# Kernel optimization log

Hardware: AMD Instinct MI355X
Metric: run time of the kernel (lower is better)

## Reference

```python
import jax, jax.numpy as jnp
import numpy as np

INPUT_NC = 512
N_HEADS = 16
D_KEY = 64
SCALE = D_KEY ** 0.5


def setup_inputs() -> dict:
    key = jax.random.key(0)
    k1, k2, k3, k4, k5, k6 = jax.random.split(key, 6)
    bs, d_seq = 8, 1024
    v = jax.random.normal(k1, (bs, d_seq, INPUT_NC), dtype=jnp.float32)
    # key-padding mask, True = masked out; broadcast over heads and query dim
    pad_mask = jax.random.bernoulli(k2, 0.1, (bs, 1, 1, d_seq))
    # fc1: input_nc -> 2*n_heads*d_key (fused K,Q projection)
    W1 = jax.random.normal(k3, (INPUT_NC, 2 * N_HEADS * D_KEY), dtype=jnp.float32) * (1.0 / np.sqrt(INPUT_NC))
    b1 = jax.random.normal(k4, (2 * N_HEADS * D_KEY,), dtype=jnp.float32) * 0.01
    # fc2: n_heads*input_nc -> input_nc
    W2 = jax.random.normal(k5, (N_HEADS * INPUT_NC, INPUT_NC), dtype=jnp.float32) * (1.0 / np.sqrt(N_HEADS * INPUT_NC))
    b2 = jax.random.normal(k6, (INPUT_NC,), dtype=jnp.float32) * 0.01
    return {"v": v, "pad_mask": pad_mask, "W1": W1, "b1": b1, "W2": W2, "b2": b2}


def reference(v, pad_mask, W1, b1, W2, b2):
    bs, d_seq, nc = v.shape
    # fused KQ projection: [bs, S, 2*H*dk] -> [bs, H, S, 2*dk]
    kq = (v @ W1 + b1).reshape(bs, d_seq, N_HEADS, 2 * D_KEY).transpose(0, 2, 1, 3)
    k, q = kq[..., :D_KEY], kq[..., D_KEY:]  # chunk: k first, q second
    attn = jnp.einsum('bhqd,bhkd->bhqk', q, k) / SCALE
    attn = jnp.where(pad_mask, jnp.float32(-1000.0), attn)
    attn = jax.nn.softmax(attn, axis=3)
    # AV with unprojected v broadcast across heads: [bs, H, S, nc]
    out = jnp.einsum('bhqk,bkc->bhqc', attn, v)
    out = out.transpose(0, 2, 1, 3).reshape(bs, d_seq, N_HEADS * nc)
    out = out @ W2 + b2
    return (out, attn)
```

## Files before the change

kernel.cpp:

```cpp
#include <hip/hip_runtime.h>


typedef __attribute__((ext_vector_type(8))) short bf16x8;
typedef __attribute__((ext_vector_type(4))) float f32x4;
typedef __attribute__((ext_vector_type(4))) unsigned short u16x4;

__device__ __forceinline__ unsigned short f2bf(float f) {
  unsigned u = __builtin_bit_cast(unsigned, f);
  u += 0x7FFFu + ((u >> 16) & 1u);
  return (unsigned short)(u >> 16);
}
__device__ __forceinline__ float bf2f(unsigned short u) {
  return __builtin_bit_cast(float, (unsigned)u << 16);
}

__device__ __forceinline__ void gload_lds16(const unsigned short* g, unsigned short* l) {
  __builtin_amdgcn_global_load_lds(
      (const __attribute__((address_space(1))) unsigned int*)(g),
      (__attribute__((address_space(3))) unsigned int*)(l), 16, 0, 0);
}


__global__ void cvt_bf16_kernel(const float* __restrict__ in,
                                unsigned short* __restrict__ out, int n4) {
  int i = blockIdx.x * blockDim.x + threadIdx.x;
  if (i >= n4) return;
  f32x4 v = reinterpret_cast<const f32x4*>(in)[i];
  u16x4 o;
#pragma unroll
  for (int j = 0; j < 4; ++j) o[j] = f2bf(v[j]);
  reinterpret_cast<u16x4*>(out)[i] = o;
}

__global__ void transpose_cvt_kernel(const float* __restrict__ in,
                                     unsigned short* __restrict__ out,
                                     int R, int C) {
  __shared__ float tile[32][33];
  int c0 = blockIdx.x * 32, r0 = blockIdx.y * 32;
  int tx = threadIdx.x & 31, ty = threadIdx.x >> 5;
#pragma unroll
  for (int i = ty; i < 32; i += 8)
    tile[i][tx] = in[(size_t)(r0 + i) * C + (c0 + tx)];
  __syncthreads();
#pragma unroll
  for (int i = ty; i < 32; i += 8)
    out[(size_t)(c0 + i) * R + (r0 + tx)] = f2bf(tile[tx][i]);
}

__launch_bounds__(256)
__global__ void gemm1_kernel(const unsigned short* __restrict__ vbf,
                             const unsigned short* __restrict__ w1t,
                             const float* __restrict__ b1,
                             unsigned short* __restrict__ q_ws,
                             unsigned short* __restrict__ k_ws) {
  const int m0 = blockIdx.y * 128, n0 = blockIdx.x * 128;
  const int w = threadIdx.x >> 6, l = threadIdx.x & 63;
  const int wr = w >> 1, wc = w & 1, lr = l & 15, lg = l >> 4;
  f32x4 acc[4][4];
#pragma unroll
  for (int mi = 0; mi < 4; ++mi)
#pragma unroll
    for (int ni = 0; ni < 4; ++ni) acc[mi][ni] = (f32x4){0.f, 0.f, 0.f, 0.f};

  for (int k0 = 0; k0 < 512; k0 += 32) {
    bf16x8 a[4], bb[4];
#pragma unroll
    for (int mi = 0; mi < 4; ++mi)
      a[mi] = *reinterpret_cast<const bf16x8*>(
          vbf + (size_t)(m0 + wr * 64 + mi * 16 + lr) * 512 + k0 + lg * 8);
#pragma unroll
    for (int ni = 0; ni < 4; ++ni)
      bb[ni] = *reinterpret_cast<const bf16x8*>(
          w1t + (size_t)(n0 + wc * 64 + ni * 16 + lr) * 512 + k0 + lg * 8);
#pragma unroll
    for (int mi = 0; mi < 4; ++mi)
#pragma unroll
      for (int ni = 0; ni < 4; ++ni)
        acc[mi][ni] = __builtin_amdgcn_mfma_f32_16x16x32_bf16(a[mi], bb[ni], acc[mi][ni], 0, 0, 0);
  }
#pragma unroll
  for (int mi = 0; mi < 4; ++mi)
#pragma unroll
    for (int ni = 0; ni < 4; ++ni) {
      int col = n0 + wc * 64 + ni * 16 + lr;
      int h = col >> 7, j = col & 127;
      float bias = b1[col];
#pragma unroll
      for (int r = 0; r < 4; ++r) {
        int row = m0 + wr * 64 + mi * 16 + lg * 4 + r;
        int bb_ = row >> 10, s = row & 1023;
        unsigned short bv = f2bf(acc[mi][ni][r] + bias);
        size_t base = ((size_t)(bb_ * 16 + h) << 16) + (size_t)s * 64;
        if (j < 64) k_ws[base + j] = bv;
        else        q_ws[base + j - 64] = bv;
      }
    }
}

__launch_bounds__(512)
__global__ void scores_kernel(const unsigned short* __restrict__ q_ws,
                              const unsigned short* __restrict__ k_ws,
                              const int* __restrict__ pad,
                              float* __restrict__ attn_out) {
  const int wg = (blockIdx.x & 7) * 512 + (blockIdx.x >> 3);
  const int qt = wg & 31, h = (wg >> 5) & 15, b = wg >> 9;
  const int bh = b * 16 + h, q0 = qt * 32;
  const int w = threadIdx.x >> 6, l = threadIdx.x & 63;
  const int lr = l & 15, lg = l >> 4;

  __shared__ unsigned short E_lds[32][1032];
  __shared__ float lw[8][32];
  __shared__ float linv_s[32];

  const unsigned short* qb = q_ws + ((size_t)bh << 16);
  const unsigned short* kb = k_ws + ((size_t)bh << 16);
  const int* pmb = pad + b * 1024;

  bf16x8 a_q[2][2];
#pragma unroll
  for (int mf = 0; mf < 2; ++mf)
#pragma unroll
    for (int ks = 0; ks < 2; ++ks)
      a_q[mf][ks] = *reinterpret_cast<const bf16x8*>(
          qb + (size_t)(q0 + mf * 16 + lr) * 64 + ks * 32 + lg * 8);

  float l_run[2][4];
#pragma unroll
  for (int mf = 0; mf < 2; ++mf)
#pragma unroll
    for (int r = 0; r < 4; ++r) l_run[mf][r] = 0.f;

#pragma unroll
  for (int sub = 0; sub < 2; ++sub) {
    const int c0 = w * 128 + sub * 64;
    f32x4 s[2][4];
#pragma unroll
    for (int mf = 0; mf < 2; ++mf)
#pragma unroll
      for (int nf = 0; nf < 4; ++nf) s[mf][nf] = (f32x4){0.f, 0.f, 0.f, 0.f};
#pragma unroll
    for (int ks = 0; ks < 2; ++ks) {
      bf16x8 bk[4];
#pragma unroll
      for (int nf = 0; nf < 4; ++nf)
        bk[nf] = *reinterpret_cast<const bf16x8*>(
            kb + (size_t)(c0 + nf * 16 + lr) * 64 + ks * 32 + lg * 8);
#pragma unroll
      for (int mf = 0; mf < 2; ++mf)
#pragma unroll
        for (int nf = 0; nf < 4; ++nf)
          s[mf][nf] = __builtin_amdgcn_mfma_f32_16x16x32_bf16(a_q[mf][ks], bk[nf], s[mf][nf], 0, 0, 0);
    }
    int msk[4];
#pragma unroll
    for (int nf = 0; nf < 4; ++nf) msk[nf] = pmb[c0 + nf * 16 + lr];
#pragma unroll
    for (int mf = 0; mf < 2; ++mf)
#pragma unroll
      for (int nf = 0; nf < 4; ++nf)
#pragma unroll
        for (int r = 0; r < 4; ++r) {
          float e = msk[nf] ? 0.f : __expf(s[mf][nf][r] * 0.125f);
          l_run[mf][r] += e;
          E_lds[mf * 16 + lg * 4 + r][c0 + nf * 16 + lr] = f2bf(e);
        }
  }

#pragma unroll
  for (int mf = 0; mf < 2; ++mf)
#pragma unroll
    for (int r = 0; r < 4; ++r) {
      float v = l_run[mf][r];
      v += __shfl_xor(v, 1); v += __shfl_xor(v, 2);
      v += __shfl_xor(v, 4); v += __shfl_xor(v, 8);
      if (lr == 0) lw[w][mf * 16 + lg * 4 + r] = v;
    }
  __syncthreads();
  if (threadIdx.x < 32) {
    float s = 0.f;
#pragma unroll
    for (int ww = 0; ww < 8; ++ww) s += lw[ww][threadIdx.x];
    linv_s[threadIdx.x] = 1.f / s;
  }
  __syncthreads();

  {
    float* attn_b = attn_out + ((size_t)bh << 20) + (size_t)q0 * 1024;
    const int row = threadIdx.x >> 4;
    const int cb = threadIdx.x & 15;
    const float sc = linv_s[row];
    float* rowp = attn_b + (size_t)row * 1024;
#pragma unroll
    for (int i = 0; i < 8; ++i) {
      int c8 = (cb + i * 16) * 8;
      bf16x8 ev = *reinterpret_cast<const bf16x8*>(&E_lds[row][c8]);
      f32x4 o0, o1;
#pragma unroll
      for (int j = 0; j < 4; ++j) o0[j] = bf2f((unsigned short)ev[j]) * sc;
#pragma unroll
      for (int j = 0; j < 4; ++j) o1[j] = bf2f((unsigned short)ev[4 + j]) * sc;
      *reinterpret_cast<f32x4*>(rowp + c8) = o0;
      *reinterpret_cast<f32x4*>(rowp + c8 + 4) = o1;
    }
  }
}

__launch_bounds__(256)
__global__ void pv_kernel(const float* __restrict__ attn,
                          const unsigned short* __restrict__ vt,
                          unsigned short* __restrict__ o_ws) {
  const int wg = (blockIdx.x & 7) * 512 + (blockIdx.x >> 3);
  const int nt = wg & 3, mt = (wg >> 2) & 7, bh = wg >> 5;
  const int b = bh >> 4, h = bh & 15;
  const int m0 = mt * 128, n0 = nt * 128;

  __shared__ unsigned short Asm[2][128 * 32];
  __shared__ unsigned short Bsm[2][128 * 32];
  const int w = threadIdx.x >> 6, l = threadIdx.x & 63;
  const int wr = w >> 1, wc = w & 1, lr = l & 15, lg = l >> 4;

  f32x4 acc[4][4];
#pragma unroll
  for (int mi = 0; mi < 4; ++mi)
#pragma unroll
    for (int ni = 0; ni < 4; ++ni) acc[mi][ni] = (f32x4){0.f, 0.f, 0.f, 0.f};

  const int srowA = threadIdx.x >> 1;
  const int kh = (threadIdx.x & 1) * 16;
  const float* gA = attn + ((size_t)bh << 20) + (size_t)(m0 + srowA) * 1024 + kh;
  unsigned short* ldsA = &Asm[0][srowA * 32 + kh];

  const int srowB = threadIdx.x >> 2;
  const int scolB = (threadIdx.x & 3) * 8;
  const unsigned short* gB0 = vt + (size_t)(n0 + srowB) * 8192 + (size_t)b * 1024 + scolB;
  const unsigned short* gB1 = vt + (size_t)(n0 + 64 + srowB) * 8192 + (size_t)b * 1024 + scolB;
  const int ldsoffB = w * 512;

  auto STAGE_B = [&](int buf, int kt) {
    int k0 = kt * 32;
    gload_lds16(gB0 + k0, &Bsm[buf][ldsoffB]);
    gload_lds16(gB1 + k0, &Bsm[buf][64 * 32 + ldsoffB]);
  };
  f32x4 ar0, ar1, ar2, ar3;
  auto LOAD_A = [&](int kt) {
    const f32x4* p = reinterpret_cast<const f32x4*>(gA + kt * 32);
    ar0 = p[0]; ar1 = p[1]; ar2 = p[2]; ar3 = p[3];
  };
  auto WRITE_A = [&](int buf) {
    bf16x8 v0, v1;
#pragma unroll
    for (int j = 0; j < 4; ++j) { v0[j] = (short)f2bf(ar0[j]); v0[4 + j] = (short)f2bf(ar1[j]); }
#pragma unroll
    for (int j = 0; j < 4; ++j) { v1[j] = (short)f2bf(ar2[j]); v1[4 + j] = (short)f2bf(ar3[j]); }
    *reinterpret_cast<bf16x8*>(ldsA + buf * 128 * 32) = v0;
    *reinterpret_cast<bf16x8*>(ldsA + buf * 128 * 32 + 8) = v1;
  };
  auto COMPUTE = [&](int buf) {
    bf16x8 a[4], bb[4];
#pragma unroll
    for (int mi = 0; mi < 4; ++mi)
      a[mi] = *reinterpret_cast<const bf16x8*>(&Asm[buf][(wr * 64 + mi * 16 + lr) * 32 + lg * 8]);
#pragma unroll
    for (int ni = 0; ni < 4; ++ni)
      bb[ni] = *reinterpret_cast<const bf16x8*>(&Bsm[buf][(wc * 64 + ni * 16 + lr) * 32 + lg * 8]);
    __builtin_amdgcn_s_setprio(1);
#pragma unroll
    for (int mi = 0; mi < 4; ++mi)
#pragma unroll
      for (int ni = 0; ni < 4; ++ni)
        acc[mi][ni] = __builtin_amdgcn_mfma_f32_16x16x32_bf16(a[mi], bb[ni], acc[mi][ni], 0, 0, 0);
    __builtin_amdgcn_s_setprio(0);
  };

  LOAD_A(0);
  STAGE_B(0, 0);
  WRITE_A(0);
  __syncthreads();
  int cur = 0;
  for (int kt = 0; kt < 31; ++kt) {
    STAGE_B(cur ^ 1, kt + 1);
    LOAD_A(kt + 1);
    COMPUTE(cur);
    WRITE_A(cur ^ 1);
    __syncthreads();
    cur ^= 1;
  }
  COMPUTE(cur);

#pragma unroll
  for (int mi = 0; mi < 4; ++mi)
#pragma unroll
    for (int ni = 0; ni < 4; ++ni)
#pragma unroll
      for (int r = 0; r < 4; ++r) {
        int row = m0 + wr * 64 + mi * 16 + lg * 4 + r;
        int col = n0 + wc * 64 + ni * 16 + lr;
        o_ws[(size_t)(b * 1024 + row) * 8192 + h * 512 + col] = f2bf(acc[mi][ni][r]);
      }
}

__launch_bounds__(256)
__global__ void gemm2_kernel(const unsigned short* __restrict__ o_ws,
                             const unsigned short* __restrict__ w2t,
                             const float* __restrict__ b2,
                             float* __restrict__ y) {
  __shared__ unsigned short As[2][64 * 32];
  __shared__ unsigned short Bs[2][128 * 32];
  const int m0 = blockIdx.y * 64, n0 = blockIdx.x * 128;
  const int w = threadIdx.x >> 6, l = threadIdx.x & 63;
  const int wr = w >> 1, wc = w & 1, lr = l & 15, lg = l >> 4;

  f32x4 acc[2][4];
#pragma unroll
  for (int mi = 0; mi < 2; ++mi)
#pragma unroll
    for (int ni = 0; ni < 4; ++ni) acc[mi][ni] = (f32x4){0.f, 0.f, 0.f, 0.f};

  const int srow = threadIdx.x >> 2;
  const int scol = (threadIdx.x & 3) * 8;
  const unsigned short* gA = o_ws + (size_t)(m0 + srow) * 8192 + scol;
  const unsigned short* gB0 = w2t + (size_t)(n0 + srow) * 8192 + scol;
  const unsigned short* gB1 = w2t + (size_t)(n0 + 64 + srow) * 8192 + scol;
  const int ldsoff = w * 512;

  auto STAGE = [&](int buf, int kt) {
    int k0 = kt * 32;
    gload_lds16(gA + k0, &As[buf][ldsoff]);
    gload_lds16(gB0 + k0, &Bs[buf][ldsoff]);
    gload_lds16(gB1 + k0, &Bs[buf][64 * 32 + ldsoff]);
  };

  auto COMPUTE = [&](int buf) {
    bf16x8 a[2], bb[4];
#pragma unroll
    for (int mi = 0; mi < 2; ++mi)
      a[mi] = *reinterpret_cast<const bf16x8*>(&As[buf][(wr * 32 + mi * 16 + lr) * 32 + lg * 8]);
#pragma unroll
    for (int ni = 0; ni < 4; ++ni)
      bb[ni] = *reinterpret_cast<const bf16x8*>(&Bs[buf][(wc * 64 + ni * 16 + lr) * 32 + lg * 8]);
    __builtin_amdgcn_s_setprio(1);
#pragma unroll
    for (int mi = 0; mi < 2; ++mi)
#pragma unroll
      for (int ni = 0; ni < 4; ++ni)
        acc[mi][ni] = __builtin_amdgcn_mfma_f32_16x16x32_bf16(a[mi], bb[ni], acc[mi][ni], 0, 0, 0);
    __builtin_amdgcn_s_setprio(0);
  };

  STAGE(0, 0);
  __syncthreads();
  int cur = 0;
  for (int kt = 0; kt < 255; ++kt) {
    STAGE(cur ^ 1, kt + 1);
    COMPUTE(cur);
    __syncthreads();
    cur ^= 1;
  }
  COMPUTE(cur);

#pragma unroll
  for (int mi = 0; mi < 2; ++mi)
#pragma unroll
    for (int ni = 0; ni < 4; ++ni) {
      int col = n0 + wc * 64 + ni * 16 + lr;
      float bias = b2[col];
#pragma unroll
      for (int r = 0; r < 4; ++r)
        y[(size_t)(m0 + wr * 32 + mi * 16 + lg * 4 + r) * 512 + col] = acc[mi][ni][r] + bias;
    }
}

extern "C" void kernel_launch(void* const* d_in, const int* in_sizes, int n_in,
                              void* d_out, int out_size, void* d_ws, size_t ws_size,
                              hipStream_t stream) {
  const float* v   = (const float*)d_in[0];
  const int*   pad = (const int*)d_in[1];
  const float* W1  = (const float*)d_in[2];
  const float* b1  = (const float*)d_in[3];
  const float* W2  = (const float*)d_in[4];
  const float* b2  = (const float*)d_in[5];
  float* out  = (float*)d_out;
  float* attn = out + (size_t)8 * 1024 * 512;

  char* ws = (char*)d_ws;
  unsigned short* w1t  = (unsigned short*)(ws);
  unsigned short* w2t  = (unsigned short*)(ws + 2097152);
  unsigned short* vt   = (unsigned short*)(ws + 10485760);
  unsigned short* vbf  = (unsigned short*)(ws + 18874368);
  unsigned short* q_ws = (unsigned short*)(ws + 27262976);
  unsigned short* k_ws = (unsigned short*)(ws + 44040192);
  unsigned short* o_ws = (unsigned short*)(ws + 60817408);

  transpose_cvt_kernel<<<dim3(64, 16), 256, 0, stream>>>(W1, w1t, 512, 2048);
  transpose_cvt_kernel<<<dim3(16, 256), 256, 0, stream>>>(W2, w2t, 8192, 512);
  transpose_cvt_kernel<<<dim3(16, 256), 256, 0, stream>>>(v, vt, 8192, 512);
  cvt_bf16_kernel<<<4096, 256, 0, stream>>>(v, vbf, 1048576);
  gemm1_kernel<<<dim3(16, 64), 256, 0, stream>>>(vbf, w1t, b1, q_ws, k_ws);
  scores_kernel<<<4096, 512, 0, stream>>>(q_ws, k_ws, pad, attn);
  pv_kernel<<<4096, 256, 0, stream>>>(attn, vt, o_ws);
  gemm2_kernel<<<dim3(4, 128), 256, 0, stream>>>(o_ws, w2t, b2, out);
}
```

Before: 738.1 us.

## Widen gemm2 tiles with swizzled grid; pack bf16 conversion in pv A staging

gemm2 now uses 64x256 output tiles on a 1D grid of 256 workgroups, with a blockIdx swizzle so that neighbouring workgroups share W2 columns. Each A tile is therefore reused across twice as many columns, at the cost of more accumulator registers and fewer workgroups. In pv_kernel, the fp32 attention load is remapped so each wave stages contiguous 16-row slabs, and rounding to bf16 uses the packed v_cvt_pk_bf16_f32 instruction instead of manual rounding. This cuts the ALU work of the conversion, but the rounding behaviour may differ slightly.

```diff
diff --git a/kernel.cpp b/kernel.cpp
--- a/kernel.cpp
+++ b/kernel.cpp
@@ -4,6 +4,7 @@
 typedef __attribute__((ext_vector_type(8))) short bf16x8;
 typedef __attribute__((ext_vector_type(4))) float f32x4;
 typedef __attribute__((ext_vector_type(4))) unsigned short u16x4;
+typedef __attribute__((ext_vector_type(4))) unsigned int u32x4;
 
 __device__ __forceinline__ unsigned short f2bf(float f) {
   unsigned u = __builtin_bit_cast(unsigned, f);
@@ -12,6 +13,11 @@
 }
 __device__ __forceinline__ float bf2f(unsigned short u) {
   return __builtin_bit_cast(float, (unsigned)u << 16);
+}
+__device__ __forceinline__ unsigned pk2(float lo, float hi) {
+  unsigned r;
+  asm volatile("v_cvt_pk_bf16_f32 %0, %1, %2" : "=v"(r) : "v"(lo), "v"(hi));
+  return r;
 }
 
 __device__ __forceinline__ void gload_lds16(const unsigned short* g, unsigned short* l) {
@@ -225,10 +231,10 @@
 #pragma unroll
     for (int ni = 0; ni < 4; ++ni) acc[mi][ni] = (f32x4){0.f, 0.f, 0.f, 0.f};
 
-  const int srowA = threadIdx.x >> 1;
-  const int kh = (threadIdx.x & 1) * 16;
-  const float* gA = attn + ((size_t)bh << 20) + (size_t)(m0 + srowA) * 1024 + kh;
-  unsigned short* ldsA = &Asm[0][srowA * 32 + kh];
+  const float* gA1 = attn + ((size_t)bh << 20)
+                   + (size_t)(m0 + w * 32 + (l >> 2)) * 1024 + (l & 3) * 8;
+  const float* gA2 = gA1 + (size_t)16 * 1024;
+  unsigned short* ldsA = &Asm[0][w * 1024 + l * 8];
 
   const int srowB = threadIdx.x >> 2;
   const int scolB = (threadIdx.x & 3) * 8;
@@ -243,17 +249,18 @@
   };
   f32x4 ar0, ar1, ar2, ar3;
   auto LOAD_A = [&](int kt) {
-    const f32x4* p = reinterpret_cast<const f32x4*>(gA + kt * 32);
-    ar0 = p[0]; ar1 = p[1]; ar2 = p[2]; ar3 = p[3];
+    const f32x4* p1 = reinterpret_cast<const f32x4*>(gA1 + kt * 32);
+    const f32x4* p2 = reinterpret_cast<const f32x4*>(gA2 + kt * 32);
+    ar0 = p1[0]; ar1 = p1[1]; ar2 = p2[0]; ar3 = p2[1];
   };
   auto WRITE_A = [&](int buf) {
-    bf16x8 v0, v1;
-#pragma unroll
-    for (int j = 0; j < 4; ++j) { v0[j] = (short)f2bf(ar0[j]); v0[4 + j] = (short)f2bf(ar1[j]); }
-#pragma unroll
-    for (int j = 0; j < 4; ++j) { v1[j] = (short)f2bf(ar2[j]); v1[4 + j] = (short)f2bf(ar3[j]); }
-    *reinterpret_cast<bf16x8*>(ldsA + buf * 128 * 32) = v0;
-    *reinterpret_cast<bf16x8*>(ldsA + buf * 128 * 32 + 8) = v1;
+    u32x4 v0, v1;
+    v0[0] = pk2(ar0[0], ar0[1]); v0[1] = pk2(ar0[2], ar0[3]);
+    v0[2] = pk2(ar1[0], ar1[1]); v0[3] = pk2(ar1[2], ar1[3]);
+    v1[0] = pk2(ar2[0], ar2[1]); v1[1] = pk2(ar2[2], ar2[3]);
+    v1[2] = pk2(ar3[0], ar3[1]); v1[3] = pk2(ar3[2], ar3[3]);
+    *reinterpret_cast<u32x4*>(ldsA + buf * 4096) = v0;
+    *reinterpret_cast<u32x4*>(ldsA + buf * 4096 + 512) = v1;
   };
   auto COMPUTE = [&](int buf) {
     bf16x8 a[4], bb[4];
@@ -304,23 +311,28 @@
                              const unsigned short* __restrict__ w2t,
                              const float* __restrict__ b2,
                              float* __restrict__ y) {
+  const int wg = (blockIdx.x & 7) * 32 + (blockIdx.x >> 3);
+  const int nt = wg >> 7, mt = wg & 127;
+  const int m0 = mt * 64, n0 = nt * 256;
+
   __shared__ unsigned short As[2][64 * 32];
-  __shared__ unsigned short Bs[2][128 * 32];
-  const int m0 = blockIdx.y * 64, n0 = blockIdx.x * 128;
+  __shared__ unsigned short Bs[2][256 * 32];
   const int w = threadIdx.x >> 6, l = threadIdx.x & 63;
   const int wr = w >> 1, wc = w & 1, lr = l & 15, lg = l >> 4;
 
-  f32x4 acc[2][4];
+  f32x4 acc[2][8];
 #pragma unroll
   for (int mi = 0; mi < 2; ++mi)
 #pragma unroll
-    for (int ni = 0; ni < 4; ++ni) acc[mi][ni] = (f32x4){0.f, 0.f, 0.f, 0.f};
+    for (int ni = 0; ni < 8; ++ni) acc[mi][ni] = (f32x4){0.f, 0.f, 0.f, 0.f};
 
   const int srow = threadIdx.x >> 2;
   const int scol = (threadIdx.x & 3) * 8;
-  const unsigned short* gA = o_ws + (size_t)(m0 + srow) * 8192 + scol;
+  const unsigned short* gA  = o_ws + (size_t)(m0 + srow) * 8192 + scol;
   const unsigned short* gB0 = w2t + (size_t)(n0 + srow) * 8192 + scol;
-  const unsigned short* gB1 = w2t + (size_t)(n0 + 64 + srow) * 8192 + scol;
+  const unsigned short* gB1 = gB0 + (size_t)64 * 8192;
+  const unsigned short* gB2 = gB0 + (size_t)128 * 8192;
+  const unsigned short* gB3 = gB0 + (size_t)192 * 8192;
   const int ldsoff = w * 512;
 
   auto STAGE = [&](int buf, int kt) {
@@ -328,21 +340,23 @@
     gload_lds16(gA + k0, &As[buf][ldsoff]);
     gload_lds16(gB0 + k0, &Bs[buf][ldsoff]);
     gload_lds16(gB1 + k0, &Bs[buf][64 * 32 + ldsoff]);
+    gload_lds16(gB2 + k0, &Bs[buf][128 * 32 + ldsoff]);
+    gload_lds16(gB3 + k0, &Bs[buf][192 * 32 + ldsoff]);
   };
 
   auto COMPUTE = [&](int buf) {
-    bf16x8 a[2], bb[4];
+    bf16x8 a[2], bb[8];
 #pragma unroll
     for (int mi = 0; mi < 2; ++mi)
       a[mi] = *reinterpret_cast<const bf16x8*>(&As[buf][(wr * 32 + mi * 16 + lr) * 32 + lg * 8]);
 #pragma unroll
-    for (int ni = 0; ni < 4; ++ni)
-      bb[ni] = *reinterpret_cast<const bf16x8*>(&Bs[buf][(wc * 64 + ni * 16 + lr) * 32 + lg * 8]);
+    for (int ni = 0; ni < 8; ++ni)
+      bb[ni] = *reinterpret_cast<const bf16x8*>(&Bs[buf][(wc * 128 + ni * 16 + lr) * 32 + lg * 8]);
     __builtin_amdgcn_s_setprio(1);
 #pragma unroll
     for (int mi = 0; mi < 2; ++mi)
 #pragma unroll
-      for (int ni = 0; ni < 4; ++ni)
+      for (int ni = 0; ni < 8; ++ni)
         acc[mi][ni] = __builtin_amdgcn_mfma_f32_16x16x32_bf16(a[mi], bb[ni], acc[mi][ni], 0, 0, 0);
     __builtin_amdgcn_s_setprio(0);
   };
@@ -361,8 +375,8 @@
 #pragma unroll
   for (int mi = 0; mi < 2; ++mi)
 #pragma unroll
-    for (int ni = 0; ni < 4; ++ni) {
-      int col = n0 + wc * 64 + ni * 16 + lr;
+    for (int ni = 0; ni < 8; ++ni) {
+      int col = n0 + wc * 128 + ni * 16 + lr;
       float bias = b2[col];
 #pragma unroll
       for (int r = 0; r < 4; ++r)
@@ -398,5 +412,5 @@
   gemm1_kernel<<<dim3(16, 64), 256, 0, stream>>>(vbf, w1t, b1, q_ws, k_ws);
   scores_kernel<<<4096, 512, 0, stream>>>(q_ws, k_ws, pad, attn);
   pv_kernel<<<4096, 256, 0, stream>>>(attn, vt, o_ws);
-  gemm2_kernel<<<dim3(4, 128), 256, 0, stream>>>(o_ws, w2t, b2, out);
-}
+  gemm2_kernel<<<256, 256, 0, stream>>>(o_ws, w2t, b2, out);
+}
```

Result: slower. 836.0 us (+13.3%).

## Feed PV GEMM from bf16 unnormalized exponentials and apply row scale in epilogue

Applied to the files above, without the earlier changes.

The scores kernel now also writes the unnormalized bf16 exponentials and the per-row inverse sums to workspace. The PV kernel reads that bf16 copy through direct global-to-LDS loads instead of reloading the fp32 attention matrix and converting it in registers, then applies the row normalization when storing its output. This halves PV's A-operand read traffic and removes the register conversion path, at the cost of an extra bf16 write in the scores kernel. The gemm2 grid is also flattened with a block-index swizzle to improve cache locality.

```diff
diff --git a/kernel.cpp b/kernel.cpp
--- a/kernel.cpp
+++ b/kernel.cpp
@@ -101,7 +101,9 @@
 __global__ void scores_kernel(const unsigned short* __restrict__ q_ws,
                               const unsigned short* __restrict__ k_ws,
                               const int* __restrict__ pad,
-                              float* __restrict__ attn_out) {
+                              float* __restrict__ attn_out,
+                              unsigned short* __restrict__ eb,
+                              float* __restrict__ linv_ws) {
   const int wg = (blockIdx.x & 7) * 512 + (blockIdx.x >> 3);
   const int qt = wg & 31, h = (wg >> 5) & 15, b = wg >> 9;
   const int bh = b * 16 + h, q0 = qt * 32;
@@ -180,7 +182,9 @@
     float s = 0.f;
 #pragma unroll
     for (int ww = 0; ww < 8; ++ww) s += lw[ww][threadIdx.x];
-    linv_s[threadIdx.x] = 1.f / s;
+    float li = 1.f / s;
+    linv_s[threadIdx.x] = li;
+    linv_ws[(size_t)bh * 1024 + q0 + threadIdx.x] = li;
   }
   __syncthreads();
 
@@ -190,6 +194,7 @@
     const int cb = threadIdx.x & 15;
     const float sc = linv_s[row];
     float* rowp = attn_b + (size_t)row * 1024;
+    unsigned short* ebrow = eb + ((size_t)bh << 20) + (size_t)(q0 + row) * 1024;
 #pragma unroll
     for (int i = 0; i < 8; ++i) {
       int c8 = (cb + i * 16) * 8;
@@ -201,13 +206,15 @@
       for (int j = 0; j < 4; ++j) o1[j] = bf2f((unsigned short)ev[4 + j]) * sc;
       *reinterpret_cast<f32x4*>(rowp + c8) = o0;
       *reinterpret_cast<f32x4*>(rowp + c8 + 4) = o1;
+      *reinterpret_cast<bf16x8*>(ebrow + c8) = ev;
     }
   }
 }
 
 __launch_bounds__(256)
-__global__ void pv_kernel(const float* __restrict__ attn,
+__global__ void pv_kernel(const unsigned short* __restrict__ eb,
                           const unsigned short* __restrict__ vt,
+                          const float* __restrict__ linv_ws,
                           unsigned short* __restrict__ o_ws) {
   const int wg = (blockIdx.x & 7) * 512 + (blockIdx.x >> 3);
   const int nt = wg & 3, mt = (wg >> 2) & 7, bh = wg >> 5;
@@ -225,35 +232,29 @@
 #pragma unroll
     for (int ni = 0; ni < 4; ++ni) acc[mi][ni] = (f32x4){0.f, 0.f, 0.f, 0.f};
 
-  const int srowA = threadIdx.x >> 1;
-  const int kh = (threadIdx.x & 1) * 16;
-  const float* gA = attn + ((size_t)bh << 20) + (size_t)(m0 + srowA) * 1024 + kh;
-  unsigned short* ldsA = &Asm[0][srowA * 32 + kh];
-
-  const int srowB = threadIdx.x >> 2;
-  const int scolB = (threadIdx.x & 3) * 8;
-  const unsigned short* gB0 = vt + (size_t)(n0 + srowB) * 8192 + (size_t)b * 1024 + scolB;
-  const unsigned short* gB1 = vt + (size_t)(n0 + 64 + srowB) * 8192 + (size_t)b * 1024 + scolB;
-  const int ldsoffB = w * 512;
-
-  auto STAGE_B = [&](int buf, int kt) {
+  const int srow = threadIdx.x >> 2;
+  const int scol = (threadIdx.x & 3) * 8;
+  const unsigned short* gA0 = eb + ((size_t)bh << 20) + (size_t)(m0 + srow) * 1024 + scol;
+  const unsigned short* gA1 = gA0 + (size_t)64 * 1024;
+  const unsigned short* gB0 = vt + (size_t)(n0 + srow) * 8192 + (size_t)b * 1024 + scol;
+  const unsigned short* gB1 = gB0 + (size_t)64 * 8192;
+  const int ldsoff = w * 512;
+
+  float linv_r[4][4];
+  {
+    const float* lrow = linv_ws + (size_t)bh * 1024 + m0 + wr * 64 + lg * 4;
+#pragma unroll
+    for (int mi = 0; mi < 4; ++mi)
+#pragma unroll
+      for (int r = 0; r < 4; ++r) linv_r[mi][r] = lrow[mi * 16 + r];
+  }
+
+  auto STAGE = [&](int buf, int kt) {
     int k0 = kt * 32;
-    gload_lds16(gB0 + k0, &Bsm[buf][ldsoffB]);
-    gload_lds16(gB1 + k0, &Bsm[buf][64 * 32 + ldsoffB]);
-  };
-  f32x4 ar0, ar1, ar2, ar3;
-  auto LOAD_A = [&](int kt) {
-    const f32x4* p = reinterpret_cast<const f32x4*>(gA + kt * 32);
-    ar0 = p[0]; ar1 = p[1]; ar2 = p[2]; ar3 = p[3];
-  };
-  auto WRITE_A = [&](int buf) {
-    bf16x8 v0, v1;
-#pragma unroll
-    for (int j = 0; j < 4; ++j) { v0[j] = (short)f2bf(ar0[j]); v0[4 + j] = (short)f2bf(ar1[j]); }
-#pragma unroll
-    for (int j = 0; j < 4; ++j) { v1[j] = (short)f2bf(ar2[j]); v1[4 + j] = (short)f2bf(ar3[j]); }
-    *reinterpret_cast<bf16x8*>(ldsA + buf * 128 * 32) = v0;
-    *reinterpret_cast<bf16x8*>(ldsA + buf * 128 * 32 + 8) = v1;
+    gload_lds16(gA0 + k0, &Asm[buf][ldsoff]);
+    gload_lds16(gA1 + k0, &Asm[buf][64 * 32 + ldsoff]);
+    gload_lds16(gB0 + k0, &Bsm[buf][ldsoff]);
+    gload_lds16(gB1 + k0, &Bsm[buf][64 * 32 + ldsoff]);
   };
   auto COMPUTE = [&](int buf) {
     bf16x8 a[4], bb[4];
@@ -272,16 +273,12 @@
     __builtin_amdgcn_s_setprio(0);
   };
 
-  LOAD_A(0);
-  STAGE_B(0, 0);
-  WRITE_A(0);
+  STAGE(0, 0);
   __syncthreads();
   int cur = 0;
   for (int kt = 0; kt < 31; ++kt) {
-    STAGE_B(cur ^ 1, kt + 1);
-    LOAD_A(kt + 1);
+    STAGE(cur ^ 1, kt + 1);
     COMPUTE(cur);
-    WRITE_A(cur ^ 1);
     __syncthreads();
     cur ^= 1;
   }
@@ -295,7 +292,8 @@
       for (int r = 0; r < 4; ++r) {
         int row = m0 + wr * 64 + mi * 16 + lg * 4 + r;
         int col = n0 + wc * 64 + ni * 16 + lr;
-        o_ws[(size_t)(b * 1024 + row) * 8192 + h * 512 + col] = f2bf(acc[mi][ni][r]);
+        o_ws[(size_t)(b * 1024 + row) * 8192 + h * 512 + col] =
+            f2bf(acc[mi][ni][r] * linv_r[mi][r]);
       }
 }
 
@@ -304,9 +302,12 @@
                              const unsigned short* __restrict__ w2t,
                              const float* __restrict__ b2,
                              float* __restrict__ y) {
+  const int wg = (blockIdx.x & 7) * 64 + (blockIdx.x >> 3);
+  const int nt = wg >> 7, mt = wg & 127;
+  const int m0 = mt * 64, n0 = nt * 128;
+
   __shared__ unsigned short As[2][64 * 32];
   __shared__ unsigned short Bs[2][128 * 32];
-  const int m0 = blockIdx.y * 64, n0 = blockIdx.x * 128;
   const int w = threadIdx.x >> 6, l = threadIdx.x & 63;
   const int wr = w >> 1, wc = w & 1, lr = l & 15, lg = l >> 4;
 
@@ -318,9 +319,9 @@
 
   const int srow = threadIdx.x >> 2;
   const int scol = (threadIdx.x & 3) * 8;
-  const unsigned short* gA = o_ws + (size_t)(m0 + srow) * 8192 + scol;
+  const unsigned short* gA  = o_ws + (size_t)(m0 + srow) * 8192 + scol;
   const unsigned short* gB0 = w2t + (size_t)(n0 + srow) * 8192 + scol;
-  const unsigned short* gB1 = w2t + (size_t)(n0 + 64 + srow) * 8192 + scol;
+  const unsigned short* gB1 = gB0 + (size_t)64 * 8192;
   const int ldsoff = w * 512;
 
   auto STAGE = [&](int buf, int kt) {
@@ -390,13 +391,15 @@
   unsigned short* q_ws = (unsigned short*)(ws + 27262976);
   unsigned short* k_ws = (unsigned short*)(ws + 44040192);
   unsigned short* o_ws = (unsigned short*)(ws + 60817408);
+  unsigned short* eb   = (unsigned short*)(ws + 195035136);
+  float*          linv = (float*)(ws + 463470592);
 
   transpose_cvt_kernel<<<dim3(64, 16), 256, 0, stream>>>(W1, w1t, 512, 2048);
   transpose_cvt_kernel<<<dim3(16, 256), 256, 0, stream>>>(W2, w2t, 8192, 512);
   transpose_cvt_kernel<<<dim3(16, 256), 256, 0, stream>>>(v, vt, 8192, 512);
   cvt_bf16_kernel<<<4096, 256, 0, stream>>>(v, vbf, 1048576);
   gemm1_kernel<<<dim3(16, 64), 256, 0, stream>>>(vbf, w1t, b1, q_ws, k_ws);
-  scores_kernel<<<4096, 512, 0, stream>>>(q_ws, k_ws, pad, attn);
-  pv_kernel<<<4096, 256, 0, stream>>>(attn, vt, o_ws);
-  gemm2_kernel<<<dim3(4, 128), 256, 0, stream>>>(o_ws, w2t, b2, out);
-}
+  scores_kernel<<<4096, 512, 0, stream>>>(q_ws, k_ws, pad, attn, eb, linv);
+  pv_kernel<<<4096, 256, 0, stream>>>(eb, vt, linv, o_ws);
+  gemm2_kernel<<<512, 256, 0, stream>>>(o_ws, w2t, b2, out);
+}
```

Result: faster. 700.6 us (-5.1%).
